# Optimization experiments

Hardware: AMD Instinct MI355X
Metric: run time of the kernel (lower is better)

The kernel has to match this reference:

```python
import jax, jax.numpy as jnp
import numpy as np

N, E = 50000, 800000
IN_DIM, HID, OUT = 128, 64, 64
NEG_SLOPE = 0.2  # PyG GATConv default leaky_relu slope


def glorot(key, shape):
    fan_in, fan_out = shape[0], shape[-1]
    lim = jnp.sqrt(6.0 / (fan_in + fan_out))
    return jax.random.uniform(key, shape, minval=-lim, maxval=lim, dtype=jnp.float32)


def setup_inputs() -> dict:
    key = jax.random.key(0)
    ks = jax.random.split(key, 10)
    x = jax.random.normal(ks[0], (N, IN_DIM), dtype=jnp.float32)
    edge_index = jax.random.randint(ks[1], (2, E), 0, N, dtype=jnp.int64)
    # GATConv layer 1: heads=2, concat=False
    W1 = glorot(ks[2], (IN_DIM, 2 * HID))
    att_src1 = glorot(ks[3], (1, 2, HID))[0]   # [2, HID]
    att_dst1 = glorot(ks[4], (1, 2, HID))[0]
    b1 = jnp.zeros((HID,), jnp.float32)
    # GATConv layer 2: heads=1, concat=False
    W2 = glorot(ks[5], (HID, OUT))
    att_src2 = glorot(ks[6], (1, 1, OUT))[0]   # [1, OUT]
    att_dst2 = glorot(ks[7], (1, 1, OUT))[0]
    b2 = jnp.zeros((OUT,), jnp.float32)
    return {"x": x, "edge_index": edge_index, "W1": W1, "att_src1": att_src1,
            "att_dst1": att_dst1, "b1": b1, "W2": W2, "att_src2": att_src2,
            "att_dst2": att_dst2, "b2": b2}


def gat_conv(x, src, dst, W, att_src, att_dst, bias, heads, out_ch):
    n = x.shape[0]
    h = (x @ W).reshape(n, heads, out_ch)              # [N,H,C]
    a_src = jnp.einsum('nhc,hc->nh', h, att_src)       # [N,H]
    a_dst = jnp.einsum('nhc,hc->nh', h, att_dst)
    e = jax.nn.leaky_relu(a_src[src] + a_dst[dst], NEG_SLOPE)  # [E,H]
    # softmax over incoming edges per destination node (stable)
    e_max = jax.ops.segment_max(e, dst, num_segments=n)
    ex = jnp.exp(e - e_max[dst])
    denom = jax.ops.segment_sum(ex, dst, num_segments=n)
    alpha = ex / (denom[dst] + 1e-16)                  # [E,H]
    msg = h[src] * alpha[:, :, None]                   # [E,H,C]
    out = jax.ops.segment_sum(msg, dst, num_segments=n)
    return out.mean(axis=1) + bias                     # concat=False -> head mean


def reference(x, edge_index, W1, att_src1, att_dst1, b1, W2, att_src2, att_dst2, b2):
    n = x.shape[0]
    loop = jnp.arange(n, dtype=edge_index.dtype)
    src = jnp.concatenate([edge_index[0], loop])       # PyG add_self_loops
    dst = jnp.concatenate([edge_index[1], loop])
    x1 = gat_conv(x, src, dst, W1, att_src1, att_dst1, b1, 2, HID)
    x1 = jax.nn.elu(x1)
    # eval mode: dropedge and dropout are identity
    out = gat_conv(x1, src, dst, W2, att_src2, att_dst2, b2, 1, OUT)
    return out
```

## Files before the change

kernel.cpp:

```cpp
#include <hip/hip_runtime.h>
#include <math.h>

#define IN_DIM 128
#define HID 64
#define NEG_SLOPE 0.2f
#define CHUNK 4096
#define GCAP 6144
#define SMEM_UNION 53248

typedef __attribute__((ext_vector_type(8))) short bf16x8;
typedef __attribute__((ext_vector_type(4))) float f32x4;
typedef __attribute__((ext_vector_type(2))) float v2f;

__device__ __forceinline__ float wmax(float v){
  #pragma unroll
  for (int o = 32; o > 0; o >>= 1) v = fmaxf(v, __shfl_xor(v, o));
  return v;
}
__device__ __forceinline__ float wsum(float v){
  #pragma unroll
  for (int o = 32; o > 0; o >>= 1) v += __shfl_xor(v, o);
  return v;
}
__device__ __forceinline__ unsigned short f2bf(float f){
  union { float f; unsigned u; } v; v.f = f;
  unsigned r = v.u + 0x7fffu + ((v.u >> 16) & 1u);
  return (unsigned short)(r >> 16);
}
__device__ __forceinline__ float bl(unsigned u){
  union { unsigned u; float f; } v; v.u = u << 16; return v.f;
}
__device__ __forceinline__ float bh(unsigned u){
  union { unsigned u; float f; } v; v.u = u & 0xffff0000u; return v.f;
}
__device__ __forceinline__ v2f up2(unsigned u){
  v2f r; r[0] = bl(u); r[1] = bh(u); return r;
}

__device__ __forceinline__ void incl_scan256(int* sh, int tid){
  #pragma unroll
  for (int off = 1; off < 256; off <<= 1){
    int v = sh[tid];
    if (tid >= off) v += sh[tid - off];
    __syncthreads();
    sh[tid] = v;
    __syncthreads();
  }
}


__device__ void scatter_body(char* smem, const unsigned* __restrict__ packed, int E,
                             const int* __restrict__ binCnt, int* __restrict__ binOff,
                             unsigned* __restrict__ binned, int bx){
  int* ib = (int*)smem;
  int* bc = ib;
  int* lh = ib + 256;
  int* lbase = ib + 512;
  int* gpos = ib + 768;
  int* lcur = ib + 1024;
  unsigned* buf = (unsigned*)(ib + 1280);
  int tid = threadIdx.x;
  int cg = binCnt[tid];
  bc[tid] = cg;
  lh[tid] = 0;
  __syncthreads();
  incl_scan256(bc, tid);
  int binBase_t = bc[tid] - cg;
  int base = bx * CHUNK;
  int rem = E - base;
  unsigned v[CHUNK / 256];
  #pragma unroll
  for (int j = 0; j < CHUNK / 256; j++){
    int i = j * 256 + tid;
    if (i < rem){ v[j] = packed[base + i]; atomicAdd(&lh[v[j] >> 24], 1); }
  }
  __syncthreads();
  lbase[tid] = lh[tid]; __syncthreads();
  incl_scan256(lbase, tid);
  int myExcl = tid ? lbase[tid - 1] : 0;
  __syncthreads();
  lbase[tid] = myExcl;
  lcur[tid] = myExcl;
  if (lh[tid] > 0) gpos[tid] = binBase_t + atomicAdd(&binOff[tid], lh[tid]);
  __syncthreads();
  #pragma unroll
  for (int j = 0; j < CHUNK / 256; j++){
    int i = j * 256 + tid;
    if (i < rem){
      int b = v[j] >> 24;
      int p = atomicAdd(&lcur[b], 1);
      buf[p] = v[j];
    }
  }
  __syncthreads();
  int cn = rem < CHUNK ? rem : CHUNK;
  for (int i = tid; i < cn; i += 256){
    unsigned u = buf[i];
    int b = u >> 24;
    binned[gpos[b] + (i - lbase[b])] = u;
  }
}

__device__ void group_body(char* smem, const unsigned* __restrict__ binned,
                           const int* __restrict__ binCnt, unsigned* __restrict__ sorted,
                           int* __restrict__ row_ptr, int N, int g){
  unsigned* A = (unsigned*)smem;
  unsigned* B = A + GCAP;
  int* ib = (int*)(B + GCAP);
  int* sc = ib;
  int* h2 = ib + 256;
  int* rs = ib + 512;
  int* cur = ib + 768;
  int tid = threadIdx.x;
  int cg = binCnt[tid];
  sc[tid] = cg;
  h2[tid] = 0;
  __syncthreads();
  incl_scan256(sc, tid);
  int base = sc[g] - binCnt[g];
  int cnt = binCnt[g]; if (cnt > GCAP) cnt = GCAP;
  __syncthreads();
  for (int i = tid; i < cnt; i += 256){
    unsigned u = binned[base + i];
    A[i] = u;
    atomicAdd(&h2[(u >> 16) & 255], 1);
  }
  __syncthreads();
  rs[tid] = h2[tid]; __syncthreads();
  incl_scan256(rs, tid);
  int excl = tid ? rs[tid - 1] : 0;
  __syncthreads();
  rs[tid] = excl; cur[tid] = excl;
  int d = g * 256 + tid;
  if (d < N) row_ptr[d] = base + excl;
  __syncthreads();
  for (int i = tid; i < cnt; i += 256){
    unsigned u = A[i];
    int p = atomicAdd(&cur[(u >> 16) & 255], 1);
    B[p] = u;
  }
  __syncthreads();
  for (int i = tid; i < cnt; i += 256)
    sorted[base + i] = B[i];
}

__device__ void gemm1_body(char* smem, const float* __restrict__ X,
                           const unsigned short* __restrict__ Wt,
                           const float* __restrict__ asrc, const float* __restrict__ adst,
                           unsigned short* __restrict__ Hb, float* __restrict__ aa,
                           int n_rows, int n0){
  const int KP = 136, CP = 132;
  unsigned short* xa = (unsigned short*)smem;
  unsigned short* wl = xa + 64 * KP;
  int tid = threadIdx.x;
  for (int idx = tid; idx < 64 * 32; idx += 256){
    int n = idx >> 5, k4 = idx & 31;
    float4 v = make_float4(0.f, 0.f, 0.f, 0.f);
    if (n0 + n < n_rows) v = *(const float4*)&X[(size_t)(n0 + n) * 128 + k4 * 4];
    ushort4 pk; pk.x = f2bf(v.x); pk.y = f2bf(v.y); pk.z = f2bf(v.z); pk.w = f2bf(v.w);
    *(ushort4*)&xa[n * KP + k4 * 4] = pk;
  }
  for (int idx = tid; idx < 128 * 16; idx += 256){
    int n = idx >> 4, k8 = idx & 15;
    uint4 v = *(const uint4*)&Wt[(size_t)n * 128 + k8 * 8];
    *(uint4*)&wl[n * KP + k8 * 8] = v;
  }
  __syncthreads();

  int lane = tid & 63, w = tid >> 6;
  int m = lane & 15, q = lane >> 4;
  f32x4 acc[4][2];
  #pragma unroll
  for (int i = 0; i < 4; i++)
    #pragma unroll
    for (int j = 0; j < 2; j++)
      #pragma unroll
      for (int r = 0; r < 4; r++) acc[i][j][r] = 0.f;
  #pragma unroll
  for (int ks = 0; ks < 4; ks++){
    bf16x8 bg[2];
    #pragma unroll
    for (int j = 0; j < 2; j++)
      bg[j] = *(const bf16x8*)&wl[((2 * w + j) * 16 + m) * KP + ks * 32 + q * 8];
    #pragma unroll
    for (int i = 0; i < 4; i++){
      bf16x8 af = *(const bf16x8*)&xa[(i * 16 + m) * KP + ks * 32 + q * 8];
      #pragma unroll
      for (int j = 0; j < 2; j++)
        acc[i][j] = __builtin_amdgcn_mfma_f32_16x16x32_bf16(af, bg[j], acc[i][j], 0, 0, 0);
    }
  }
  __syncthreads();
  float* C = (float*)smem;
  #pragma unroll
  for (int i = 0; i < 4; i++)
    #pragma unroll
    for (int j = 0; j < 2; j++)
      #pragma unroll
      for (int r = 0; r < 4; r++)
        C[(i * 16 + q * 4 + r) * CP + (2 * w + j) * 16 + m] = acc[i][j][r];
  __syncthreads();

  int row = tid >> 2;
  int c0 = (tid & 3) * 32;
  int n = n0 + row;
  int head = (tid & 3) >> 1;
  float s_p = 0.f, d_p = 0.f;
  unsigned short hb[32];
  #pragma unroll
  for (int c = 0; c < 32; c += 4){
    f32x4 v = *(const f32x4*)&C[row * CP + c0 + c];
    #pragma unroll
    for (int u = 0; u < 4; u++){
      int ch = (c0 + c + u) & 63;
      s_p += v[u] * asrc[head * 64 + ch];
      d_p += v[u] * adst[head * 64 + ch];
      hb[c + u] = f2bf(v[u]);
    }
  }
  if (n < n_rows){
    #pragma unroll
    for (int c = 0; c < 32; c += 8){
      uint4 pk;
      pk.x = (unsigned)hb[c]     | ((unsigned)hb[c + 1] << 16);
      pk.y = (unsigned)hb[c + 2] | ((unsigned)hb[c + 3] << 16);
      pk.z = (unsigned)hb[c + 4] | ((unsigned)hb[c + 5] << 16);
      pk.w = (unsigned)hb[c + 6] | ((unsigned)hb[c + 7] << 16);
      *(uint4*)&Hb[(size_t)n * 128 + c0 + c] = pk;
    }
  }
  s_p += __shfl_xor(s_p, 1);
  d_p += __shfl_xor(d_p, 1);
  if ((tid & 1) == 0 && n < n_rows){
    aa[(size_t)n * 4 + head]     = s_p;
    aa[(size_t)n * 4 + 2 + head] = d_p;
  }
}


__global__ __launch_bounds__(256) void sort_gemm_a(const unsigned* __restrict__ packed, int E,
    const int* __restrict__ binCnt, int* __restrict__ binOff, unsigned* __restrict__ binned,
    int NS, const float* __restrict__ X, const unsigned short* __restrict__ W1t,
    const float* __restrict__ asrc1, const float* __restrict__ adst1,
    unsigned short* __restrict__ h1b, float* __restrict__ aa1, int n_rows){
  __shared__ char smem[SMEM_UNION];
  int bx = blockIdx.x;
  if (bx < NS){
    scatter_body(smem, packed, E, binCnt, binOff, binned, bx);
  } else {
    gemm1_body(smem, X, W1t, asrc1, adst1, h1b, aa1, n_rows, (bx - NS) * 64);
  }
}

__global__ __launch_bounds__(256) void sort_gemm_b(const unsigned* __restrict__ binned,
    const int* __restrict__ binCnt, unsigned* __restrict__ sorted, int* __restrict__ row_ptr,
    int N, int NS, int gofs, const float* __restrict__ X, const unsigned short* __restrict__ W1t,
    const float* __restrict__ asrc1, const float* __restrict__ adst1,
    unsigned short* __restrict__ h1b, float* __restrict__ aa1, int n_rows){
  __shared__ char smem[SMEM_UNION];
  int bx = blockIdx.x;
  if (bx < NS){
    group_body(smem, binned, binCnt, sorted, row_ptr, N, bx);
  } else {
    gemm1_body(smem, X, W1t, asrc1, adst1, h1b, aa1, n_rows, (gofs + bx - NS) * 64);
  }
}


__global__ __launch_bounds__(256) void prep(const int* __restrict__ ei, int E, int NBLK,
                                            unsigned* __restrict__ packed,
                                            int* __restrict__ binCnt,
                                            const float* __restrict__ W1,
                                            const float* __restrict__ W2,
                                            unsigned short* __restrict__ W1t,
                                            unsigned short* __restrict__ W2t,
                                            int* __restrict__ row_ptr, int N){
  int tid = threadIdx.x;
  if ((int)blockIdx.x < NBLK){
    __shared__ int lh[256];
    lh[tid] = 0; __syncthreads();
    int base = blockIdx.x * CHUNK;
    #pragma unroll
    for (int j = 0; j < CHUNK / 256; j++){
      int e = base + j * 256 + tid;
      if (e < E){
        unsigned s = (unsigned)ei[e];
        unsigned d = (unsigned)ei[E + e];
        packed[e] = (d << 16) | s;
        atomicAdd(&lh[d >> 8], 1);
      }
    }
    __syncthreads();
    if (lh[tid] > 0) atomicAdd(&binCnt[tid], lh[tid]);
  } else {
    int t = (blockIdx.x - NBLK) * 256 + tid;
    if (t < 128 * 128){
      int n = t >> 7, k = t & 127;
      W1t[n * 128 + k] = f2bf(W1[k * 128 + n]);
    }
    int t2 = t - 128 * 128;
    if (t2 >= 0 && t2 < 64 * 64){
      int n = t2 >> 6, k = t2 & 63;
      W2t[n * 64 + k] = f2bf(W2[k * 64 + n]);
    }
    if (t == 0) row_ptr[N] = E;
  }
}


template<int K, int NC, int HEADS>
__global__ __launch_bounds__(512) void gemm_mfma(const float* __restrict__ X,
    const unsigned short* __restrict__ Wt, const float* __restrict__ asrc,
    const float* __restrict__ adst, unsigned short* __restrict__ Hb,
    float* __restrict__ aa, int n_rows)
{
  constexpr int MT = 128;
  constexpr int KP = K + 8;
  constexpr int CP = NC + 4;
  constexpr int MF = MT / 16;
  constexpr int NFt = NC / 16;
  constexpr int WPN = 8 / NFt;
  constexpr int MFW = MF / WPN;
  constexpr unsigned SM1 = (unsigned)(MT + NC) * KP * 2;
  constexpr unsigned SM2 = (unsigned)MT * CP * 4;
  __shared__ char smem[SM1 > SM2 ? SM1 : SM2];
  unsigned short* xa = (unsigned short*)smem;
  unsigned short* wl = xa + MT * KP;
  int tid = threadIdx.x;
  int n0 = blockIdx.x * MT;

  for (int idx = tid; idx < MT * (K / 4); idx += 512){
    int n = idx / (K / 4), k4 = idx % (K / 4);
    float4 v = make_float4(0.f, 0.f, 0.f, 0.f);
    if (n0 + n < n_rows) v = *(const float4*)&X[(size_t)(n0 + n) * K + k4 * 4];
    ushort4 pk; pk.x = f2bf(v.x); pk.y = f2bf(v.y); pk.z = f2bf(v.z); pk.w = f2bf(v.w);
    *(ushort4*)&xa[n * KP + k4 * 4] = pk;
  }
  for (int idx = tid; idx < NC * (K / 8); idx += 512){
    int n = idx / (K / 8), k8 = idx % (K / 8);
    uint4 v = *(const uint4*)&Wt[(size_t)n * K + k8 * 8];
    *(uint4*)&wl[n * KP + k8 * 8] = v;
  }
  __syncthreads();

  int lane = tid & 63, w = tid >> 6;
  int m = lane & 15, q = lane >> 4;
  int nf = w % NFt;
  int mseg = w / NFt;
  f32x4 acc[MFW];
  #pragma unroll
  for (int i = 0; i < MFW; i++)
    #pragma unroll
    for (int r = 0; r < 4; r++) acc[i][r] = 0.f;

  #pragma unroll
  for (int ks = 0; ks < K / 32; ks++){
    bf16x8 bg = *(const bf16x8*)&wl[(nf * 16 + m) * KP + ks * 32 + q * 8];
    #pragma unroll
    for (int i = 0; i < MFW; i++){
      bf16x8 af = *(const bf16x8*)&xa[((mseg * MFW + i) * 16 + m) * KP + ks * 32 + q * 8];
      acc[i] = __builtin_amdgcn_mfma_f32_16x16x32_bf16(af, bg, acc[i], 0, 0, 0);
    }
  }
  __syncthreads();
  float* C = (float*)smem;
  #pragma unroll
  for (int i = 0; i < MFW; i++)
    #pragma unroll
    for (int r = 0; r < 4; r++)
      C[((mseg * MFW + i) * 16 + q * 4 + r) * CP + nf * 16 + m] = acc[i][r];
  __syncthreads();

  constexpr int CH = NC / 4;
  int row = tid >> 2;
  int c0 = (tid & 3) * CH;
  int n = n0 + row;
  int head = (HEADS == 2) ? (c0 >> 6) : 0;
  float s_p = 0.f, d_p = 0.f;
  unsigned short hb[CH];
  #pragma unroll
  for (int c = 0; c < CH; c += 4){
    f32x4 v = *(const f32x4*)&C[row * CP + c0 + c];
    #pragma unroll
    for (int u = 0; u < 4; u++){
      int ch = (c0 + c + u) & 63;
      s_p += v[u] * asrc[head * 64 + ch];
      d_p += v[u] * adst[head * 64 + ch];
      hb[c + u] = f2bf(v[u]);
    }
  }
  if (n < n_rows){
    #pragma unroll
    for (int c = 0; c < CH; c += 8){
      uint4 pk;
      pk.x = (unsigned)hb[c]     | ((unsigned)hb[c + 1] << 16);
      pk.y = (unsigned)hb[c + 2] | ((unsigned)hb[c + 3] << 16);
      pk.z = (unsigned)hb[c + 4] | ((unsigned)hb[c + 5] << 16);
      pk.w = (unsigned)hb[c + 6] | ((unsigned)hb[c + 7] << 16);
      *(uint4*)&Hb[(size_t)n * NC + c0 + c] = pk;
    }
  }
  s_p += __shfl_xor(s_p, 1);
  d_p += __shfl_xor(d_p, 1);
  if (HEADS == 2){
    if ((tid & 1) == 0 && n < n_rows){
      aa[(size_t)n * 4 + head]     = s_p;
      aa[(size_t)n * 4 + 2 + head] = d_p;
    }
  } else {
    s_p += __shfl_xor(s_p, 2);
    d_p += __shfl_xor(d_p, 2);
    if ((tid & 3) == 0 && n < n_rows){
      aa[(size_t)n * 2]     = s_p;
      aa[(size_t)n * 2 + 1] = d_p;
    }
  }
}


__global__ void agg_layer1(const int* __restrict__ row_ptr, const unsigned* __restrict__ sorted,
                           const float* __restrict__ aa, const unsigned short* __restrict__ h1b,
                           const float* __restrict__ b1, float* __restrict__ x1, int n_nodes){
  int d = (blockIdx.x * blockDim.x + threadIdx.x) >> 6;
  int lane = threadIdx.x & 63;
  if (d >= n_nodes) return;
  int rp0 = row_ptr[d];
  int deg = row_ptr[d + 1] - rp0;
  float2 adv = *(const float2*)&aa[d * 4 + 2];
  int s = -1;
  if (lane < deg) s = (int)(sorted[rp0 + lane] & 0xffffu);
  else if (lane == deg) s = d;
  float e0 = -INFINITY, e1 = -INFINITY;
  if (s >= 0){
    float2 asv = *(const float2*)&aa[s * 4];
    float t0 = asv.x + adv.x;
    float t1 = asv.y + adv.y;
    e0 = t0 >= 0.f ? t0 : NEG_SLOPE * t0;
    e1 = t1 >= 0.f ? t1 : NEG_SLOPE * t1;
  }
  float m0 = wmax(e0), m1 = wmax(e1);
  float p0 = (s >= 0) ? __expf(e0 - m0) : 0.f;
  float p1 = (s >= 0) ? __expf(e1 - m1) : 0.f;
  float al0 = p0 / (wsum(p0) + 1e-16f);
  float al1 = p1 / (wsum(p1) + 1e-16f);
  int ne = deg + 1;
  int g = lane >> 4, c = lane & 15;
  v2f acc[4] = {{0.f,0.f},{0.f,0.f},{0.f,0.f},{0.f,0.f}};
  #pragma unroll 2
  for (int j0 = 0; j0 < ne; j0 += 4){
    int j = j0 + g;
    int sj = __shfl(s, j);
    float a0 = __shfl(al0, j);
    float a1 = __shfl(al1, j);
    if (j < ne){
      uint4 v = ((const uint4*)(h1b + (size_t)sj * 128))[c];
      float a = (c < 8) ? a0 : a1;
      v2f av = {a, a};
      acc[0] = av * up2(v.x) + acc[0];
      acc[1] = av * up2(v.y) + acc[1];
      acc[2] = av * up2(v.z) + acc[2];
      acc[3] = av * up2(v.w) + acc[3];
    }
  }
  float accf[8] = {acc[0][0], acc[0][1], acc[1][0], acc[1][1],
                   acc[2][0], acc[2][1], acc[3][0], acc[3][1]};
  #pragma unroll
  for (int i = 0; i < 8; i++){
    accf[i] += __shfl_xor(accf[i], 16);
    accf[i] += __shfl_xor(accf[i], 32);
  }
  float outv[8];
  #pragma unroll
  for (int i = 0; i < 8; i++){
    float o = __shfl_xor(accf[i], 8);
    outv[i] = 0.5f * (accf[i] + o);
  }
  if (g == 0 && c < 8){
    float r[8];
    #pragma unroll
    for (int i = 0; i < 8; i++){
      float v = outv[i] + b1[c * 8 + i];
      r[i] = v > 0.f ? v : expm1f(v);
    }
    float* p = &x1[(size_t)d * 64 + c * 8];
    *(float4*)p       = make_float4(r[0], r[1], r[2], r[3]);
    *(float4*)(p + 4) = make_float4(r[4], r[5], r[6], r[7]);
  }
}

__global__ void agg_layer2(const int* __restrict__ row_ptr, const unsigned* __restrict__ sorted,
                           const float* __restrict__ aa, const unsigned short* __restrict__ h2b,
                           const float* __restrict__ b2, float* __restrict__ out, int n_nodes){
  int d = (blockIdx.x * blockDim.x + threadIdx.x) >> 6;
  int lane = threadIdx.x & 63;
  if (d >= n_nodes) return;
  int rp0 = row_ptr[d];
  int deg = row_ptr[d + 1] - rp0;
  float ad = aa[d * 2 + 1];
  int s = -1;
  if (lane < deg) s = (int)(sorted[rp0 + lane] & 0xffffu);
  else if (lane == deg) s = d;
  float e = -INFINITY;
  if (s >= 0){
    float t = aa[s * 2 + 0] + ad;
    e = t >= 0.f ? t : NEG_SLOPE * t;
  }
  float m = wmax(e);
  float p = (s >= 0) ? __expf(e - m) : 0.f;
  float al = p / (wsum(p) + 1e-16f);
  int ne = deg + 1;
  int g = lane >> 3, c = lane & 7;
  v2f acc[4] = {{0.f,0.f},{0.f,0.f},{0.f,0.f},{0.f,0.f}};
  #pragma unroll 2
  for (int j0 = 0; j0 < ne; j0 += 8){
    int j = j0 + g;
    int sj = __shfl(s, j);
    float a = __shfl(al, j);
    if (j < ne){
      uint4 v = ((const uint4*)(h2b + (size_t)sj * 64))[c];
      v2f av = {a, a};
      acc[0] = av * up2(v.x) + acc[0];
      acc[1] = av * up2(v.y) + acc[1];
      acc[2] = av * up2(v.z) + acc[2];
      acc[3] = av * up2(v.w) + acc[3];
    }
  }
  float accf[8] = {acc[0][0], acc[0][1], acc[1][0], acc[1][1],
                   acc[2][0], acc[2][1], acc[3][0], acc[3][1]};
  #pragma unroll
  for (int i = 0; i < 8; i++){
    accf[i] += __shfl_xor(accf[i], 8);
    accf[i] += __shfl_xor(accf[i], 16);
    accf[i] += __shfl_xor(accf[i], 32);
  }
  if (lane < 8){
    float r[8];
    #pragma unroll
    for (int i = 0; i < 8; i++) r[i] = accf[i] + b2[lane * 8 + i];
    float* q = &out[(size_t)d * 64 + lane * 8];
    *(float4*)q       = make_float4(r[0], r[1], r[2], r[3]);
    *(float4*)(q + 4) = make_float4(r[4], r[5], r[6], r[7]);
  }
}

extern "C" void kernel_launch(void* const* d_in, const int* in_sizes, int n_in,
                              void* d_out, int out_size, void* d_ws, size_t ws_size,
                              hipStream_t stream){
  const float* x     = (const float*)d_in[0];
  const int*   ei    = (const int*)d_in[1];
  const float* W1    = (const float*)d_in[2];
  const float* asrc1 = (const float*)d_in[3];
  const float* adst1 = (const float*)d_in[4];
  const float* b1    = (const float*)d_in[5];
  const float* W2    = (const float*)d_in[6];
  const float* asrc2 = (const float*)d_in[7];
  const float* adst2 = (const float*)d_in[8];
  const float* b2    = (const float*)d_in[9];
  float* out = (float*)d_out;
  int N = in_sizes[0] / IN_DIM;
  int E = in_sizes[1] / 2;
  int NG = (N + 255) >> 8;
  int NBLK = (E + CHUNK - 1) / CHUNK;
  int ngrp = (N + 3) / 4;
  int GT = (N + 63) / 64;
  int GA = GT / 2;
  int GB = GT - GA;

  char* p = (char*)d_ws;
  unsigned short* h1b = (unsigned short*)p;  p += (size_t)N * 128 * 2;
  unsigned short* h2b = (unsigned short*)p;  p += (size_t)N * 64 * 2;
  float* x1  = (float*)p;                    p += (size_t)N * 64 * 4;
  float* aa1 = (float*)p;                    p += (size_t)N * 4 * 4;
  float* aa2 = (float*)p;                    p += (size_t)N * 2 * 4;
  unsigned* packed = (unsigned*)p;           p += (size_t)E * 4;
  unsigned* binned = (unsigned*)p;           p += (size_t)E * 4;
  unsigned* sorted = (unsigned*)p;           p += (size_t)E * 4;
  int* row_ptr   = (int*)p;                  p += (size_t)(N + 1) * 4;
  int* binCnt    = (int*)p;                  p += 256 * 4;
  int* binOff    = (int*)p;                  p += 256 * 4;
  unsigned short* W1t = (unsigned short*)p;  p += 128 * 128 * 2;
  unsigned short* W2t = (unsigned short*)p;

  hipMemsetAsync(binCnt, 0, 512 * sizeof(int), stream);
  prep<<<NBLK + 80, 256, 0, stream>>>(ei, E, NBLK, packed, binCnt,
                                      W1, W2, W1t, W2t, row_ptr, N);
  sort_gemm_a<<<NBLK + GA, 256, 0, stream>>>(packed, E, binCnt, binOff, binned,
                                             NBLK, x, W1t, asrc1, adst1, h1b, aa1, N);
  sort_gemm_b<<<NG + GB, 256, 0, stream>>>(binned, binCnt, sorted, row_ptr, N,
                                           NG, GA, x, W1t, asrc1, adst1, h1b, aa1, N);
  agg_layer1<<<ngrp, 256, 0, stream>>>(row_ptr, sorted, aa1, h1b, b1, x1, N);
  gemm_mfma<64, 64, 1><<<(N + 127) / 128, 512, 0, stream>>>(
      x1, W2t, asrc2, adst2, h2b, aa2, N);
  agg_layer2<<<ngrp, 256, 0, stream>>>(row_ptr, sorted, aa2, h2b, b2, out, N);
}
```

Measured before the change: 235.6 us.

## Reorder layer-2 GAT to aggregate before projection and refine sort bins

Layer 2 now aggregates the bf16 ELU output x1 over neighbours first and applies W2 afterwards in a new output GEMM, using linearity. The attention logits come from precomputed W2·att vectors inside agg_layer1, which removes the separate layer-2 GEMM and the fp32 x1 round trip. The edge sort switches from 256 to 512 coarse bins of 128 destinations each, which halves the group capacity and per-block work. The risk is extra bf16 rounding on x1 and on the aggregated features before the final matmul.

New measurement: 241.5 us. 2.5% more time.

```diff
diff --git a/kernel.cpp b/kernel.cpp
--- a/kernel.cpp
+++ b/kernel.cpp
@@ -5,7 +5,7 @@
 #define HID 64
 #define NEG_SLOPE 0.2f
 #define CHUNK 4096
-#define GCAP 6144
+#define GCAP 3072
 #define SMEM_UNION 53248
 
 typedef __attribute__((ext_vector_type(8))) short bf16x8;
@@ -47,47 +47,122 @@
     __syncthreads();
   }
 }
+__device__ __forceinline__ void incl_scan512(int* sh, int tid){
+  #pragma unroll
+  for (int off = 1; off < 512; off <<= 1){
+    int v0 = sh[tid];
+    int v1 = sh[tid + 256];
+    int a0 = (tid >= off) ? sh[tid - off] : 0;
+    int a1 = (tid + 256 >= off) ? sh[tid + 256 - off] : 0;
+    __syncthreads();
+    sh[tid] = v0 + a0;
+    sh[tid + 256] = v1 + a1;
+    __syncthreads();
+  }
+}
+
+
+__global__ __launch_bounds__(256) void prep(const int* __restrict__ ei, int E, int NBLK,
+                                            unsigned* __restrict__ packed,
+                                            int* __restrict__ binCnt,
+                                            const float* __restrict__ W1,
+                                            const float* __restrict__ W2,
+                                            const float* __restrict__ asrc2,
+                                            const float* __restrict__ adst2,
+                                            unsigned short* __restrict__ W1t,
+                                            unsigned short* __restrict__ W2t,
+                                            float* __restrict__ wsrc2,
+                                            float* __restrict__ wdst2,
+                                            int* __restrict__ row_ptr, int N){
+  int tid = threadIdx.x;
+  int bx = blockIdx.x;
+  if (bx < NBLK){
+    __shared__ int lh[512];
+    lh[tid] = 0; lh[tid + 256] = 0; __syncthreads();
+    int base = bx * CHUNK;
+    #pragma unroll
+    for (int j = 0; j < CHUNK / 256; j++){
+      int e = base + j * 256 + tid;
+      if (e < E){
+        unsigned s = (unsigned)ei[e];
+        unsigned d = (unsigned)ei[E + e];
+        packed[e] = (d << 16) | s;
+        atomicAdd(&lh[d >> 7], 1);
+      }
+    }
+    __syncthreads();
+    if (lh[tid] > 0) atomicAdd(&binCnt[tid], lh[tid]);
+    if (lh[tid + 256] > 0) atomicAdd(&binCnt[tid + 256], lh[tid + 256]);
+  } else if (bx < NBLK + 80){
+    int t = (bx - NBLK) * 256 + tid;
+    if (t < 128 * 128){
+      int n = t >> 7, k = t & 127;
+      W1t[n * 128 + k] = f2bf(W1[k * 128 + n]);
+    }
+    int t2 = t - 128 * 128;
+    if (t2 >= 0 && t2 < 64 * 64){
+      int n = t2 >> 6, k = t2 & 63;
+      W2t[n * 64 + k] = f2bf(W2[k * 64 + n]);
+    }
+    if (t == 0) row_ptr[N] = E;
+  } else {
+    if (tid < 64){
+      float s = 0.f, d = 0.f;
+      for (int c = 0; c < 64; c++){
+        float w = W2[tid * 64 + c];
+        s += w * asrc2[c];
+        d += w * adst2[c];
+      }
+      wsrc2[tid] = s;
+      wdst2[tid] = d;
+    }
+  }
+}
 
 
 __device__ void scatter_body(char* smem, const unsigned* __restrict__ packed, int E,
                              const int* __restrict__ binCnt, int* __restrict__ binOff,
                              unsigned* __restrict__ binned, int bx){
   int* ib = (int*)smem;
-  int* bc = ib;
-  int* lh = ib + 256;
-  int* lbase = ib + 512;
-  int* gpos = ib + 768;
-  int* lcur = ib + 1024;
-  unsigned* buf = (unsigned*)(ib + 1280);
+  int* bc    = ib;
+  int* lh    = ib + 512;
+  int* lbase = ib + 1024;
+  int* gpos  = ib + 1536;
+  int* lcur  = ib + 2048;
+  unsigned* buf = (unsigned*)(ib + 2560);
   int tid = threadIdx.x;
-  int cg = binCnt[tid];
-  bc[tid] = cg;
-  lh[tid] = 0;
-  __syncthreads();
-  incl_scan256(bc, tid);
-  int binBase_t = bc[tid] - cg;
+  int c0 = binCnt[tid], c1 = binCnt[tid + 256];
+  bc[tid] = c0; bc[tid + 256] = c1;
+  lh[tid] = 0;  lh[tid + 256] = 0;
+  __syncthreads();
+  incl_scan512(bc, tid);
+  int gbase_lo = bc[tid] - c0;
+  int gbase_hi = bc[tid + 256] - c1;
   int base = bx * CHUNK;
   int rem = E - base;
   unsigned v[CHUNK / 256];
   #pragma unroll
   for (int j = 0; j < CHUNK / 256; j++){
     int i = j * 256 + tid;
-    if (i < rem){ v[j] = packed[base + i]; atomicAdd(&lh[v[j] >> 24], 1); }
-  }
-  __syncthreads();
-  lbase[tid] = lh[tid]; __syncthreads();
-  incl_scan256(lbase, tid);
-  int myExcl = tid ? lbase[tid - 1] : 0;
-  __syncthreads();
-  lbase[tid] = myExcl;
-  lcur[tid] = myExcl;
-  if (lh[tid] > 0) gpos[tid] = binBase_t + atomicAdd(&binOff[tid], lh[tid]);
+    if (i < rem){ v[j] = packed[base + i]; atomicAdd(&lh[v[j] >> 23], 1); }
+  }
+  __syncthreads();
+  lbase[tid] = lh[tid]; lbase[tid + 256] = lh[tid + 256];
+  __syncthreads();
+  incl_scan512(lbase, tid);
+  int inc_lo = lbase[tid], inc_hi = lbase[tid + 256];
+  int cnt_lo = lh[tid], cnt_hi = lh[tid + 256];
+  __syncthreads();
+  lbase[tid] = inc_lo - cnt_lo; lbase[tid + 256] = inc_hi - cnt_hi;
+  lcur[tid]  = inc_lo - cnt_lo; lcur[tid + 256]  = inc_hi - cnt_hi;
+  if (cnt_lo > 0) gpos[tid] = gbase_lo + atomicAdd(&binOff[tid], cnt_lo);
+  if (cnt_hi > 0) gpos[tid + 256] = gbase_hi + atomicAdd(&binOff[tid + 256], cnt_hi);
   __syncthreads();
   #pragma unroll
   for (int j = 0; j < CHUNK / 256; j++){
     int i = j * 256 + tid;
     if (i < rem){
-      int b = v[j] >> 24;
+      int b = v[j] >> 23;
       int p = atomicAdd(&lcur[b], 1);
       buf[p] = v[j];
     }
@@ -96,7 +171,7 @@
   int cn = rem < CHUNK ? rem : CHUNK;
   for (int i = tid; i < cn; i += 256){
     unsigned u = buf[i];
-    int b = u >> 24;
+    int b = u >> 23;
     binned[gpos[b] + (i - lbase[b])] = u;
   }
 }
@@ -107,42 +182,44 @@
   unsigned* A = (unsigned*)smem;
   unsigned* B = A + GCAP;
   int* ib = (int*)(B + GCAP);
-  int* sc = ib;
-  int* h2 = ib + 256;
-  int* rs = ib + 512;
-  int* cur = ib + 768;
+  int* sc  = ib;
+  int* h2  = ib + 512;
+  int* rs  = ib + 768;
+  int* cur = ib + 1024;
   int tid = threadIdx.x;
-  int cg = binCnt[tid];
-  sc[tid] = cg;
+  int c0 = binCnt[tid], c1 = binCnt[tid + 256];
+  sc[tid] = c0; sc[tid + 256] = c1;
   h2[tid] = 0;
   __syncthreads();
-  incl_scan256(sc, tid);
+  incl_scan512(sc, tid);
   int base = sc[g] - binCnt[g];
   int cnt = binCnt[g]; if (cnt > GCAP) cnt = GCAP;
   __syncthreads();
   for (int i = tid; i < cnt; i += 256){
     unsigned u = binned[base + i];
     A[i] = u;
-    atomicAdd(&h2[(u >> 16) & 255], 1);
-  }
-  __syncthreads();
-  rs[tid] = h2[tid]; __syncthreads();
+    atomicAdd(&h2[(u >> 16) & 127], 1);
+  }
+  __syncthreads();
+  rs[tid] = (tid < 128) ? h2[tid] : 0;
+  __syncthreads();
   incl_scan256(rs, tid);
   int excl = tid ? rs[tid - 1] : 0;
   __syncthreads();
   rs[tid] = excl; cur[tid] = excl;
-  int d = g * 256 + tid;
-  if (d < N) row_ptr[d] = base + excl;
+  int d = g * 128 + tid;
+  if (tid < 128 && d < N) row_ptr[d] = base + excl;
   __syncthreads();
   for (int i = tid; i < cnt; i += 256){
     unsigned u = A[i];
-    int p = atomicAdd(&cur[(u >> 16) & 255], 1);
+    int p = atomicAdd(&cur[(u >> 16) & 127], 1);
     B[p] = u;
   }
   __syncthreads();
   for (int i = tid; i < cnt; i += 256)
     sorted[base + i] = B[i];
 }
+
 
 __device__ void gemm1_body(char* smem, const float* __restrict__ X,
                            const unsigned short* __restrict__ Wt,
@@ -267,160 +344,11 @@
 }
 
 
-__global__ __launch_bounds__(256) void prep(const int* __restrict__ ei, int E, int NBLK,
-                                            unsigned* __restrict__ packed,
-                                            int* __restrict__ binCnt,
-                                            const float* __restrict__ W1,
-                                            const float* __restrict__ W2,
-                                            unsigned short* __restrict__ W1t,
-                                            unsigned short* __restrict__ W2t,
-                                            int* __restrict__ row_ptr, int N){
-  int tid = threadIdx.x;
-  if ((int)blockIdx.x < NBLK){
-    __shared__ int lh[256];
-    lh[tid] = 0; __syncthreads();
-    int base = blockIdx.x * CHUNK;
-    #pragma unroll
-    for (int j = 0; j < CHUNK / 256; j++){
-      int e = base + j * 256 + tid;
-      if (e < E){
-        unsigned s = (unsigned)ei[e];
-        unsigned d = (unsigned)ei[E + e];
-        packed[e] = (d << 16) | s;
-        atomicAdd(&lh[d >> 8], 1);
-      }
-    }
-    __syncthreads();
-    if (lh[tid] > 0) atomicAdd(&binCnt[tid], lh[tid]);
-  } else {
-    int t = (blockIdx.x - NBLK) * 256 + tid;
-    if (t < 128 * 128){
-      int n = t >> 7, k = t & 127;
-      W1t[n * 128 + k] = f2bf(W1[k * 128 + n]);
-    }
-    int t2 = t - 128 * 128;
-    if (t2 >= 0 && t2 < 64 * 64){
-      int n = t2 >> 6, k = t2 & 63;
-      W2t[n * 64 + k] = f2bf(W2[k * 64 + n]);
-    }
-    if (t == 0) row_ptr[N] = E;
-  }
-}
-
-
-template<int K, int NC, int HEADS>
-__global__ __launch_bounds__(512) void gemm_mfma(const float* __restrict__ X,
-    const unsigned short* __restrict__ Wt, const float* __restrict__ asrc,
-    const float* __restrict__ adst, unsigned short* __restrict__ Hb,
-    float* __restrict__ aa, int n_rows)
-{
-  constexpr int MT = 128;
-  constexpr int KP = K + 8;
-  constexpr int CP = NC + 4;
-  constexpr int MF = MT / 16;
-  constexpr int NFt = NC / 16;
-  constexpr int WPN = 8 / NFt;
-  constexpr int MFW = MF / WPN;
-  constexpr unsigned SM1 = (unsigned)(MT + NC) * KP * 2;
-  constexpr unsigned SM2 = (unsigned)MT * CP * 4;
-  __shared__ char smem[SM1 > SM2 ? SM1 : SM2];
-  unsigned short* xa = (unsigned short*)smem;
-  unsigned short* wl = xa + MT * KP;
-  int tid = threadIdx.x;
-  int n0 = blockIdx.x * MT;
-
-  for (int idx = tid; idx < MT * (K / 4); idx += 512){
-    int n = idx / (K / 4), k4 = idx % (K / 4);
-    float4 v = make_float4(0.f, 0.f, 0.f, 0.f);
-    if (n0 + n < n_rows) v = *(const float4*)&X[(size_t)(n0 + n) * K + k4 * 4];
-    ushort4 pk; pk.x = f2bf(v.x); pk.y = f2bf(v.y); pk.z = f2bf(v.z); pk.w = f2bf(v.w);
-    *(ushort4*)&xa[n * KP + k4 * 4] = pk;
-  }
-  for (int idx = tid; idx < NC * (K / 8); idx += 512){
-    int n = idx / (K / 8), k8 = idx % (K / 8);
-    uint4 v = *(const uint4*)&Wt[(size_t)n * K + k8 * 8];
-    *(uint4*)&wl[n * KP + k8 * 8] = v;
-  }
-  __syncthreads();
-
-  int lane = tid & 63, w = tid >> 6;
-  int m = lane & 15, q = lane >> 4;
-  int nf = w % NFt;
-  int mseg = w / NFt;
-  f32x4 acc[MFW];
-  #pragma unroll
-  for (int i = 0; i < MFW; i++)
-    #pragma unroll
-    for (int r = 0; r < 4; r++) acc[i][r] = 0.f;
-
-  #pragma unroll
-  for (int ks = 0; ks < K / 32; ks++){
-    bf16x8 bg = *(const bf16x8*)&wl[(nf * 16 + m) * KP + ks * 32 + q * 8];
-    #pragma unroll
-    for (int i = 0; i < MFW; i++){
-      bf16x8 af = *(const bf16x8*)&xa[((mseg * MFW + i) * 16 + m) * KP + ks * 32 + q * 8];
-      acc[i] = __builtin_amdgcn_mfma_f32_16x16x32_bf16(af, bg, acc[i], 0, 0, 0);
-    }
-  }
-  __syncthreads();
-  float* C = (float*)smem;
-  #pragma unroll
-  for (int i = 0; i < MFW; i++)
-    #pragma unroll
-    for (int r = 0; r < 4; r++)
-      C[((mseg * MFW + i) * 16 + q * 4 + r) * CP + nf * 16 + m] = acc[i][r];
-  __syncthreads();
-
-  constexpr int CH = NC / 4;
-  int row = tid >> 2;
-  int c0 = (tid & 3) * CH;
-  int n = n0 + row;
-  int head = (HEADS == 2) ? (c0 >> 6) : 0;
-  float s_p = 0.f, d_p = 0.f;
-  unsigned short hb[CH];
-  #pragma unroll
-  for (int c = 0; c < CH; c += 4){
-    f32x4 v = *(const f32x4*)&C[row * CP + c0 + c];
-    #pragma unroll
-    for (int u = 0; u < 4; u++){
-      int ch = (c0 + c + u) & 63;
-      s_p += v[u] * asrc[head * 64 + ch];
-      d_p += v[u] * adst[head * 64 + ch];
-      hb[c + u] = f2bf(v[u]);
-    }
-  }
-  if (n < n_rows){
-    #pragma unroll
-    for (int c = 0; c < CH; c += 8){
-      uint4 pk;
-      pk.x = (unsigned)hb[c]     | ((unsigned)hb[c + 1] << 16);
-      pk.y = (unsigned)hb[c + 2] | ((unsigned)hb[c + 3] << 16);
-      pk.z = (unsigned)hb[c + 4] | ((unsigned)hb[c + 5] << 16);
-      pk.w = (unsigned)hb[c + 6] | ((unsigned)hb[c + 7] << 16);
-      *(uint4*)&Hb[(size_t)n * NC + c0 + c] = pk;
-    }
-  }
-  s_p += __shfl_xor(s_p, 1);
-  d_p += __shfl_xor(d_p, 1);
-  if (HEADS == 2){
-    if ((tid & 1) == 0 && n < n_rows){
-      aa[(size_t)n * 4 + head]     = s_p;
-      aa[(size_t)n * 4 + 2 + head] = d_p;
-    }
-  } else {
-    s_p += __shfl_xor(s_p, 2);
-    d_p += __shfl_xor(d_p, 2);
-    if ((tid & 3) == 0 && n < n_rows){
-      aa[(size_t)n * 2]     = s_p;
-      aa[(size_t)n * 2 + 1] = d_p;
-    }
-  }
-}
-
-
 __global__ void agg_layer1(const int* __restrict__ row_ptr, const unsigned* __restrict__ sorted,
                            const float* __restrict__ aa, const unsigned short* __restrict__ h1b,
-                           const float* __restrict__ b1, float* __restrict__ x1, int n_nodes){
+                           const float* __restrict__ b1, const float* __restrict__ wsrc2,
+                           const float* __restrict__ wdst2, unsigned short* __restrict__ x1b,
+                           float* __restrict__ aa2, int n_nodes){
   int d = (blockIdx.x * blockDim.x + threadIdx.x) >> 6;
   int lane = threadIdx.x & 63;
   if (d >= n_nodes) return;
@@ -476,21 +404,40 @@
     outv[i] = 0.5f * (accf[i] + o);
   }
   if (g == 0 && c < 8){
-    float r[8];
+    float xv[8];
+    unsigned short rb[8];
     #pragma unroll
     for (int i = 0; i < 8; i++){
       float v = outv[i] + b1[c * 8 + i];
-      r[i] = v > 0.f ? v : expm1f(v);
-    }
-    float* p = &x1[(size_t)d * 64 + c * 8];
-    *(float4*)p       = make_float4(r[0], r[1], r[2], r[3]);
-    *(float4*)(p + 4) = make_float4(r[4], r[5], r[6], r[7]);
-  }
-}
+      xv[i] = v > 0.f ? v : expm1f(v);
+      rb[i] = f2bf(xv[i]);
+    }
+    uint4 pk;
+    pk.x = (unsigned)rb[0] | ((unsigned)rb[1] << 16);
+    pk.y = (unsigned)rb[2] | ((unsigned)rb[3] << 16);
+    pk.z = (unsigned)rb[4] | ((unsigned)rb[5] << 16);
+    pk.w = (unsigned)rb[6] | ((unsigned)rb[7] << 16);
+    *(uint4*)&x1b[(size_t)d * 64 + c * 8] = pk;
+    float sp = 0.f, dp = 0.f;
+    #pragma unroll
+    for (int i = 0; i < 8; i++){
+      sp += xv[i] * wsrc2[c * 8 + i];
+      dp += xv[i] * wdst2[c * 8 + i];
+    }
+    sp += __shfl_xor(sp, 1); dp += __shfl_xor(dp, 1);
+    sp += __shfl_xor(sp, 2); dp += __shfl_xor(dp, 2);
+    sp += __shfl_xor(sp, 4); dp += __shfl_xor(dp, 4);
+    if (c == 0){
+      aa2[(size_t)d * 2]     = sp;
+      aa2[(size_t)d * 2 + 1] = dp;
+    }
+  }
+}
+
 
 __global__ void agg_layer2(const int* __restrict__ row_ptr, const unsigned* __restrict__ sorted,
-                           const float* __restrict__ aa, const unsigned short* __restrict__ h2b,
-                           const float* __restrict__ b2, float* __restrict__ out, int n_nodes){
+                           const float* __restrict__ aa, const unsigned short* __restrict__ x1b,
+                           unsigned short* __restrict__ aggX, int n_nodes){
   int d = (blockIdx.x * blockDim.x + threadIdx.x) >> 6;
   int lane = threadIdx.x & 63;
   if (d >= n_nodes) return;
@@ -517,7 +464,7 @@
     int sj = __shfl(s, j);
     float a = __shfl(al, j);
     if (j < ne){
-      uint4 v = ((const uint4*)(h2b + (size_t)sj * 64))[c];
+      uint4 v = ((const uint4*)(x1b + (size_t)sj * 64))[c];
       v2f av = {a, a};
       acc[0] = av * up2(v.x) + acc[0];
       acc[1] = av * up2(v.y) + acc[1];
@@ -534,12 +481,81 @@
     accf[i] += __shfl_xor(accf[i], 32);
   }
   if (lane < 8){
-    float r[8];
-    #pragma unroll
-    for (int i = 0; i < 8; i++) r[i] = accf[i] + b2[lane * 8 + i];
-    float* q = &out[(size_t)d * 64 + lane * 8];
-    *(float4*)q       = make_float4(r[0], r[1], r[2], r[3]);
-    *(float4*)(q + 4) = make_float4(r[4], r[5], r[6], r[7]);
+    unsigned short rb[8];
+    #pragma unroll
+    for (int i = 0; i < 8; i++) rb[i] = f2bf(accf[i]);
+    uint4 pk;
+    pk.x = (unsigned)rb[0] | ((unsigned)rb[1] << 16);
+    pk.y = (unsigned)rb[2] | ((unsigned)rb[3] << 16);
+    pk.z = (unsigned)rb[4] | ((unsigned)rb[5] << 16);
+    pk.w = (unsigned)rb[6] | ((unsigned)rb[7] << 16);
+    *(uint4*)&aggX[(size_t)d * 64 + lane * 8] = pk;
+  }
+}
+
+
+__global__ __launch_bounds__(512) void gemm_out(const unsigned short* __restrict__ Xb,
+    const unsigned short* __restrict__ W2t, const float* __restrict__ b2,
+    float* __restrict__ out, int n_rows){
+  const int KP = 72, CP = 68;
+  __shared__ char smem[128 * CP * 4];
+  unsigned short* xa = (unsigned short*)smem;
+  unsigned short* wl = xa + 128 * KP;
+  int tid = threadIdx.x;
+  int n0 = blockIdx.x * 128;
+  for (int idx = tid; idx < 128 * 8; idx += 512){
+    int n = idx >> 3, k8 = idx & 7;
+    uint4 v = make_uint4(0, 0, 0, 0);
+    if (n0 + n < n_rows) v = *(const uint4*)&Xb[(size_t)(n0 + n) * 64 + k8 * 8];
+    *(uint4*)&xa[n * KP + k8 * 8] = v;
+  }
+  for (int idx = tid; idx < 64 * 8; idx += 512){
+    int n = idx >> 3, k8 = idx & 7;
+    uint4 v = *(const uint4*)&W2t[(size_t)n * 64 + k8 * 8];
+    *(uint4*)&wl[n * KP + k8 * 8] = v;
+  }
+  __syncthreads();
+
+  int lane = tid & 63, w = tid >> 6;
+  int m = lane & 15, q = lane >> 4;
+  int nf = w & 3;
+  int mseg = w >> 2;
+  f32x4 acc[4];
+  #pragma unroll
+  for (int i = 0; i < 4; i++)
+    #pragma unroll
+    for (int r = 0; r < 4; r++) acc[i][r] = 0.f;
+  #pragma unroll
+  for (int ks = 0; ks < 2; ks++){
+    bf16x8 bg = *(const bf16x8*)&wl[(nf * 16 + m) * KP + ks * 32 + q * 8];
+    #pragma unroll
+    for (int i = 0; i < 4; i++){
+      bf16x8 af = *(const bf16x8*)&xa[((mseg * 4 + i) * 16 + m) * KP + ks * 32 + q * 8];
+      acc[i] = __builtin_amdgcn_mfma_f32_16x16x32_bf16(af, bg, acc[i], 0, 0, 0);
+    }
+  }
+  __syncthreads();
+  float* C = (float*)smem;
+  #pragma unroll
+  for (int i = 0; i < 4; i++)
+    #pragma unroll
+    for (int r = 0; r < 4; r++)
+      C[((mseg * 4 + i) * 16 + q * 4 + r) * CP + nf * 16 + m] = acc[i][r];
+  __syncthreads();
+
+  int row = tid >> 2, cq = tid & 3;
+  int n = n0 + row;
+  if (n < n_rows){
+    #pragma unroll
+    for (int c = 0; c < 16; c += 4){
+      f32x4 v = *(const f32x4*)&C[row * CP + cq * 16 + c];
+      float4 r;
+      r.x = v[0] + b2[cq * 16 + c];
+      r.y = v[1] + b2[cq * 16 + c + 1];
+      r.z = v[2] + b2[cq * 16 + c + 2];
+      r.w = v[3] + b2[cq * 16 + c + 3];
+      *(float4*)&out[(size_t)n * 64 + cq * 16 + c] = r;
+    }
   }
 }
 
@@ -559,7 +575,7 @@
   float* out = (float*)d_out;
   int N = in_sizes[0] / IN_DIM;
   int E = in_sizes[1] / 2;
-  int NG = (N + 255) >> 8;
+  int NG = (N + 127) >> 7;
   int NBLK = (E + CHUNK - 1) / CHUNK;
   int ngrp = (N + 3) / 4;
   int GT = (N + 63) / 64;
@@ -568,28 +584,31 @@
 
   char* p = (char*)d_ws;
   unsigned short* h1b = (unsigned short*)p;  p += (size_t)N * 128 * 2;
-  unsigned short* h2b = (unsigned short*)p;  p += (size_t)N * 64 * 2;
-  float* x1  = (float*)p;                    p += (size_t)N * 64 * 4;
+  unsigned short* x1b = (unsigned short*)p;  p += (size_t)N * 64 * 2;
+  unsigned short* aggX= (unsigned short*)p;  p += (size_t)N * 64 * 2;
   float* aa1 = (float*)p;                    p += (size_t)N * 4 * 4;
   float* aa2 = (float*)p;                    p += (size_t)N * 2 * 4;
   unsigned* packed = (unsigned*)p;           p += (size_t)E * 4;
   unsigned* binned = (unsigned*)p;           p += (size_t)E * 4;
   unsigned* sorted = (unsigned*)p;           p += (size_t)E * 4;
   int* row_ptr   = (int*)p;                  p += (size_t)(N + 1) * 4;
-  int* binCnt    = (int*)p;                  p += 256 * 4;
-  int* binOff    = (int*)p;                  p += 256 * 4;
+  int* binCnt    = (int*)p;                  p += 512 * 4;
+  int* binOff    = (int*)p;                  p += 512 * 4;
+  float* wsrc2   = (float*)p;                p += 64 * 4;
+  float* wdst2   = (float*)p;                p += 64 * 4;
   unsigned short* W1t = (unsigned short*)p;  p += 128 * 128 * 2;
   unsigned short* W2t = (unsigned short*)p;
 
-  hipMemsetAsync(binCnt, 0, 512 * sizeof(int), stream);
-  prep<<<NBLK + 80, 256, 0, stream>>>(ei, E, NBLK, packed, binCnt,
-                                      W1, W2, W1t, W2t, row_ptr, N);
+  hipMemsetAsync(binCnt, 0, 1024 * sizeof(int), stream);
+  prep<<<NBLK + 81, 256, 0, stream>>>(ei, E, NBLK, packed, binCnt,
+                                      W1, W2, asrc2, adst2, W1t, W2t,
+                                      wsrc2, wdst2, row_ptr, N);
   sort_gemm_a<<<NBLK + GA, 256, 0, stream>>>(packed, E, binCnt, binOff, binned,
                                              NBLK, x, W1t, asrc1, adst1, h1b, aa1, N);
   sort_gemm_b<<<NG + GB, 256, 0, stream>>>(binned, binCnt, sorted, row_ptr, N,
                                            NG, GA, x, W1t, asrc1, adst1, h1b, aa1, N);
-  agg_layer1<<<ngrp, 256, 0, stream>>>(row_ptr, sorted, aa1, h1b, b1, x1, N);
-  gemm_mfma<64, 64, 1><<<(N + 127) / 128, 512, 0, stream>>>(
-      x1, W2t, asrc2, adst2, h2b, aa2, N);
-  agg_layer2<<<ngrp, 256, 0, stream>>>(row_ptr, sorted, aa2, h2b, b2, out, N);
-}
+  agg_layer1<<<ngrp, 256, 0, stream>>>(row_ptr, sorted, aa1, h1b, b1,
+                                       wsrc2, wdst2, x1b, aa2, N);
+  agg_layer2<<<ngrp, 256, 0, stream>>>(row_ptr, sorted, aa2, x1b, aggX, N);
+  gemm_out<<<(N + 127) / 128, 512, 0, stream>>>(aggX, W2t, b2, out, N);
+}
```
